# Kernel tuning notes

Measured on AMD Instinct MI355X. Metric: run time of the kernel, lower is better.

Reference implementation:

```python
import jax, jax.numpy as jnp
import numpy as np

NUM_TOKENS = 2048
HIDDEN = 1024
INTER = 2048
NUM_EXPERTS = 8
TOPK = 2


def setup_inputs() -> dict:
    key = jax.random.key(0)
    k1, k2, k3, k4 = jax.random.split(key, 4)
    hidden_states = jax.random.normal(k1, (NUM_TOKENS, HIDDEN), dtype=jnp.float32)
    router_logits = jax.random.normal(k2, (NUM_TOKENS, NUM_EXPERTS), dtype=jnp.float32)
    # fc1: [E, hidden, 2*intermediate] (proj/gate for SwiGLU), fc2: [E, intermediate, hidden]
    w1 = jax.random.normal(k3, (NUM_EXPERTS, HIDDEN, 2 * INTER), dtype=jnp.float32) * 0.02
    w2 = jax.random.normal(k4, (NUM_EXPERTS, INTER, HIDDEN), dtype=jnp.float32) * 0.02
    return {"hidden_states": hidden_states, "router_logits": router_logits, "w1": w1, "w2": w2}


def _grouped_gemm(x, w, expert_ids):
    """x: [T, D], w: [E, D, O], expert_ids: [T] -> [T, O].
    Tokens are routed to expert expert_ids[t]; equivalent to the sequential
    per-expert GEMM on contiguously sorted tokens. Small fixed loop over E."""
    out = jnp.zeros((x.shape[0], w.shape[-1]), dtype=x.dtype)
    for e in range(w.shape[0]):
        mask = (expert_ids == e)[:, None]
        out = out + jnp.where(mask, x, 0.0) @ w[e]
    return out


def reference(hidden_states, router_logits, w1, w2):
    # top-k routing + softmax over the selected logits
    top_logits, top_idx = jax.lax.top_k(router_logits, TOPK)      # [N, K]
    scores = jax.nn.softmax(top_logits, axis=-1)                  # [N, K]

    flat_idx = top_idx.reshape(-1)                                # [N*K]
    sorted_indices = jnp.argsort(flat_idx)                        # permute tokens grouped by expert
    permuted = hidden_states[sorted_indices // TOPK]              # [N*K, D]
    sorted_experts = flat_idx[sorted_indices]                     # [N*K] expert id per permuted row

    fc1_out = _grouped_gemm(permuted, w1, sorted_experts)         # [N*K, 2*I]
    proj, gate = jnp.split(fc1_out, 2, axis=-1)
    act = jax.nn.silu(proj) * gate                                # SwiGLU
    expert_out = _grouped_gemm(act, w2, sorted_experts)           # [N*K, D]

    # unpermute (scatter back) and weighted combine over top-k
    unpermuted = jnp.zeros_like(expert_out).at[sorted_indices].set(expert_out)
    unpermuted = unpermuted.reshape(-1, TOPK, expert_out.shape[-1])
    return (unpermuted * scores[..., None]).sum(axis=1)           # [N, D]
```

## Files before the change

kernel.cpp:

```cpp
#include <hip/hip_runtime.h>
#include <hip/hip_bf16.h>

constexpr int T = 2048;
constexpr int H = 1024;
constexpr int I = 2048;
constexpr int N2 = 2 * I;
constexpr int RCAP = 5120;
constexpr int MAXT = 40;

constexpr int WS_OFF = 16;
constexpr int WS_TEXP = 32;
constexpr int WS_TOPKP = 4256;
constexpr int WS_ROWTOK = 8352;
constexpr int WS_TOKROW = 13472;
constexpr size_t WSB_ZROW = 114688;
constexpr size_t WSB_HSB  = 131072;
constexpr size_t WSB_ACT  = 8u << 20;
constexpr size_t WSB_PW1  = 32u << 20;
constexpr size_t WSB_PW2  = 96u << 20;

constexpr int W1T_BLKS = 8 * 32 * 16;
constexpr int W2T_BLKS = 8 * 64 * 4;
constexpr int HSB_BLKS = T * H / 2048;
constexpr int FC1_BLKS = 32 * MAXT;

typedef __attribute__((ext_vector_type(4))) float f32x4;
typedef __attribute__((ext_vector_type(8))) short s16x8;

__device__ __forceinline__ short f2bf(float f) {
    unsigned u = __float_as_uint(f);
    u += 0x7FFFu + ((u >> 16) & 1u);
    return (short)(u >> 16);
}

#define MFMA16(a, b, c) __builtin_amdgcn_mfma_f32_16x16x32_bf16(a, b, c, 0, 0, 0)

__device__ __forceinline__ void gl2lds16(const void* g, void* l) {
    __builtin_amdgcn_global_load_lds(
        (const __attribute__((address_space(1))) void*)g,
        (__attribute__((address_space(3))) void*)l, 16, 0, 0);
}

#define VM_WAIT4 asm volatile("s_waitcnt vmcnt(4)" ::: "memory")
#define VM_WAIT0 asm volatile("s_waitcnt vmcnt(0)" ::: "memory")
#define BARRIER                                     \
    do {                                            \
        asm volatile("" ::: "memory");              \
        __builtin_amdgcn_s_barrier();               \
        asm volatile("" ::: "memory");              \
    } while (0)

__global__ __launch_bounds__(256) void pre_kernel(const float* __restrict__ logits,
                                                  int* __restrict__ wsi,
                                                  float* __restrict__ wsf,
                                                  const float* __restrict__ hs,
                                                  unsigned short* __restrict__ hsb,
                                                  const float* __restrict__ w1,
                                                  unsigned short* __restrict__ pw1) {
    __shared__ __align__(16) float Lf[32 * 256];
    const int t = threadIdx.x;

    if (blockIdx.x < W1T_BLKS) {
        int b = blockIdx.x;
        int cs = b & 15, k0i = (b >> 4) & 31, e = b >> 9;
        const float* src = w1 + (size_t)e * H * N2 + (size_t)(k0i * 32) * N2 + cs * 256;
        #pragma unroll
        for (int i = 0; i < 8; i++) {
            int c = t + i * 256;
            int row = c >> 6, col4 = (c & 63) * 4;
            gl2lds16(src + (size_t)row * N2 + col4, &Lf[c * 4]);
        }
        __syncthreads();
        int gatebit = cs >> 3, csl = cs & 7;
        #pragma unroll
        for (int i = 0; i < 4; i++) {
            int cidx = t + i * 256;
            int within = cidx & 31, subh = (cidx >> 5) & 1;
            int kg = (cidx >> 6) & 3, ctp = cidx >> 8;
            int x = ctp * 64 + subh * 32 + within;
            s16x8 s;
            #pragma unroll
            for (int kk = 0; kk < 8; kk++) s[kk] = f2bf(Lf[(kg * 8 + kk) * 256 + x]);
            int n = gatebit * 32 + subh * 64 + within;
            int ct = csl * 4 + ctp;
            *(s16x8*)(pw1 + ((size_t)(e * 32 + ct) * 32 + k0i) * 4096 + (kg * 128 + n) * 8) = s;
        }
        return;
    }
    if (blockIdx.x > W1T_BLKS) {
        int i = (((int)blockIdx.x - W1T_BLKS - 1) * 256 + t) * 8;
        f32x4 a = *(const f32x4*)(hs + i);
        f32x4 b = *(const f32x4*)(hs + i + 4);
        s16x8 s = {f2bf(a[0]), f2bf(a[1]), f2bf(a[2]), f2bf(a[3]),
                   f2bf(b[0]), f2bf(b[1]), f2bf(b[2]), f2bf(b[3])};
        *(s16x8*)(hsb + i) = s;
        return;
    }

    int* cnt  = (int*)Lf;
    int* base = cnt + 8;
    int* fill = base + 9;
    if (t < 8) { cnt[t] = 0; fill[t] = 0; }
    for (int r = t; r < RCAP; r += 256) wsi[WS_ROWTOK + r] = -1;
    unsigned short* zr = (unsigned short*)((char*)wsi + WSB_ZROW);
    for (int i = t; i < H; i += 256) zr[i] = 0;
    __syncthreads();

    int e0a[8], e1a[8];
    #pragma unroll
    for (int j = 0; j < 8; j++) {
        int tok = t * 8 + j;
        const float* l = logits + tok * 8;
        float v0 = -1e30f; int i0 = 0;
        #pragma unroll
        for (int i = 0; i < 8; i++) { float v = l[i]; if (v > v0) { v0 = v; i0 = i; } }
        float v1 = -1e30f; int i1 = 0;
        #pragma unroll
        for (int i = 0; i < 8; i++) { if (i == i0) continue; float v = l[i]; if (v > v1) { v1 = v; i1 = i; } }
        float ex = __expf(v1 - v0);
        float inv = 1.f / (1.f + ex);
        wsf[WS_TOPKP + tok * 2] = inv;
        wsf[WS_TOPKP + tok * 2 + 1] = ex * inv;
        e0a[j] = i0; e1a[j] = i1;
        atomicAdd(&cnt[i0], 1);
        atomicAdd(&cnt[i1], 1);
    }
    __syncthreads();
    if (t == 0) {
        int acc = 0;
        for (int e = 0; e < 8; e++) { base[e] = acc; acc += (cnt[e] + 127) & ~127; }
        base[8] = acc;
        for (int e = 0; e < 9; e++) wsi[WS_OFF + e] = base[e];
    }
    __syncthreads();
    for (int tt = t; tt < MAXT; tt += 256) {
        int rb = tt * 128, ex = 0;
        for (int e = 0; e < 8; e++)
            if (rb >= base[e] && rb < base[e + 1]) ex = e;
        wsi[WS_TEXP + tt] = ex;
    }
    #pragma unroll
    for (int j = 0; j < 8; j++) {
        int tok = t * 8 + j;
        int ee[2] = {e0a[j], e1a[j]};
        #pragma unroll
        for (int k = 0; k < 2; k++) {
            int e = ee[k];
            int slot = atomicAdd(&fill[e], 1);
            int r = base[e] + slot;
            wsi[WS_ROWTOK + r] = tok;
            wsi[WS_TOKROW + tok * 2 + k] = r;
        }
    }
}

__global__ __launch_bounds__(256, 4) void fc1_kernel(
    const unsigned short* __restrict__ hsb, const unsigned short* __restrict__ pw1,
    const int* __restrict__ wsi, const unsigned short* __restrict__ zrow,
    unsigned short* __restrict__ act,
    const float* __restrict__ w2, unsigned short* __restrict__ pw2) {
    __shared__ __align__(16) unsigned short SM[32 * 512];
    const int t = threadIdx.x;

    if (blockIdx.x >= FC1_BLKS) {
        float* Lf = (float*)SM;
        int b = (int)blockIdx.x - FC1_BLKS;
        int cs = b & 3, k0i = (b >> 2) & 63, e = b >> 8;
        const float* src = w2 + (size_t)e * I * H + (size_t)(k0i * 32) * H + cs * 256;
        #pragma unroll
        for (int i = 0; i < 8; i++) {
            int c = t + i * 256;
            int row = c >> 6, col4 = (c & 63) * 4;
            gl2lds16(src + (size_t)row * H + col4, &Lf[c * 4]);
        }
        __syncthreads();
        #pragma unroll
        for (int i = 0; i < 4; i++) {
            int cidx = t + i * 256;
            int n = cidx & 127, kg = (cidx >> 7) & 3, h1 = cidx >> 9;
            int x = h1 * 128 + n;
            s16x8 s;
            #pragma unroll
            for (int kk = 0; kk < 8; kk++) s[kk] = f2bf(Lf[(kg * 8 + kk) * 256 + x]);
            int ht = cs * 2 + h1;
            *(s16x8*)(pw2 + ((size_t)(e * 8 + ht) * 64 + k0i) * 4096 + (kg * 128 + n) * 8) = s;
        }
        return;
    }

    unsigned short* A0 = SM;
    unsigned short* B0 = SM + 4096;
    unsigned short* A1 = SM + 8192;
    unsigned short* B1 = SM + 12288;
    const int ct = blockIdx.x & 31, rt = blockIdx.x >> 5;
    const int rowb = rt * 128;
    if (rowb >= wsi[WS_OFF + 8]) return;
    const int e = wsi[WS_TEXP + rt];
    const unsigned short* pb = pw1 + (size_t)((e * 32 + ct) * 32) * 4096;

    const int m = t & 127;
    const int tok = wsi[WS_ROWTOK + rowb + m];
    const unsigned short* rp = (tok >= 0) ? (hsb + (size_t)tok * H) : zrow;
    const int kga = t >> 7;

    const int lane = t & 63, w = t >> 6, wr = w >> 1, wc = w & 1;
    const int q = lane >> 4, l16 = lane & 15;

    f32x4 zero = {0.f, 0.f, 0.f, 0.f};
    f32x4 acc[4][4];
    #pragma unroll
    for (int mi = 0; mi < 4; mi++)
        #pragma unroll
        for (int ni = 0; ni < 4; ni++) acc[mi][ni] = zero;

    #define FC1_STAGE(k0i, Ab, Bb)                                             \
        do {                                                                   \
            const int k0_ = (k0i) * 32;                                        \
            gl2lds16(rp + k0_ + kga * 8, &(Ab)[t * 8]);                        \
            gl2lds16(rp + k0_ + (kga + 2) * 8, &(Ab)[(t + 256) * 8]);          \
            const unsigned short* ps_ = pb + (size_t)(k0i) * 4096;             \
            gl2lds16(ps_ + t * 8, &(Bb)[t * 8]);                               \
            gl2lds16(ps_ + (t + 256) * 8, &(Bb)[(t + 256) * 8]);               \
        } while (0)

    #define FC1_COMPUTE(Ab, Bb)                                                \
        do {                                                                   \
            s16x8 af[4], bf[4];                                                \
            _Pragma("unroll")                                                  \
            for (int mi = 0; mi < 4; mi++)                                     \
                af[mi] = *(const s16x8*)&(Ab)[(q * 128 + wr * 64 + mi * 16 + l16) * 8]; \
            _Pragma("unroll")                                                  \
            for (int ni = 0; ni < 4; ni++)                                     \
                bf[ni] = *(const s16x8*)&(Bb)[(q * 128 + wc * 64 + ni * 16 + l16) * 8]; \
            _Pragma("unroll")                                                  \
            for (int mi = 0; mi < 4; mi++)                                     \
                _Pragma("unroll")                                              \
                for (int ni = 0; ni < 4; ni++)                                 \
                    acc[mi][ni] = MFMA16(af[mi], bf[ni], acc[mi][ni]);         \
        } while (0)

    FC1_STAGE(0, A0, B0);
    FC1_STAGE(1, A1, B1);
    for (int k0i = 0; k0i < 30; k0i += 2) {
        VM_WAIT4;
        BARRIER;
        FC1_COMPUTE(A0, B0);
        BARRIER;
        FC1_STAGE(k0i + 2, A0, B0);
        VM_WAIT4;
        BARRIER;
        FC1_COMPUTE(A1, B1);
        BARRIER;
        FC1_STAGE(k0i + 3, A1, B1);
    }
    VM_WAIT4;
    BARRIER;
    FC1_COMPUTE(A0, B0);
    BARRIER;
    VM_WAIT0;
    BARRIER;
    FC1_COMPUTE(A1, B1);

    #pragma unroll
    for (int mi = 0; mi < 4; mi++)
        #pragma unroll
        for (int r = 0; r < 4; r++) {
            int row = rowb + wr * 64 + mi * 16 + q * 4 + r;
            #pragma unroll
            for (int ni = 0; ni < 2; ni++) {
                int col = ct * 64 + wc * 32 + ni * 16 + l16;
                float p = acc[mi][ni][r], g = acc[mi][ni + 2][r];
                float val = p * g / (1.f + __expf(-p));
                act[(size_t)row * I + col] = (unsigned short)f2bf(val);
            }
        }
}

__global__ __launch_bounds__(256, 4) void fc2_kernel(
    const unsigned short* __restrict__ act, const unsigned short* __restrict__ pw2,
    const int* __restrict__ wsi, float* __restrict__ eo) {
    __shared__ __align__(16) unsigned short SM[32 * 512];
    unsigned short* A0 = SM;
    unsigned short* B0 = SM + 4096;
    unsigned short* A1 = SM + 8192;
    unsigned short* B1 = SM + 12288;
    const int t = threadIdx.x;
    const int ht = blockIdx.x, rt = blockIdx.y, ks = blockIdx.z;
    const int rowb = rt * 128;
    if (rowb >= wsi[WS_OFF + 8]) return;
    const int e = wsi[WS_TEXP + rt];
    const unsigned short* pb = pw2 + (size_t)((e * 8 + ht) * 64) * 4096;

    const int m = t & 127;
    const unsigned short* rp = act + (size_t)(rowb + m) * I;
    const int kga = t >> 7;

    const int lane = t & 63, w = t >> 6, wr = w >> 1, wc = w & 1;
    const int q = lane >> 4, l16 = lane & 15;

    f32x4 zero = {0.f, 0.f, 0.f, 0.f};
    f32x4 acc[4][4];
    #pragma unroll
    for (int mi = 0; mi < 4; mi++)
        #pragma unroll
        for (int ni = 0; ni < 4; ni++) acc[mi][ni] = zero;

    #define FC2_STAGE(k0i, Ab, Bb)                                             \
        do {                                                                   \
            const int k0_ = (k0i) * 32;                                        \
            gl2lds16(rp + k0_ + kga * 8, &(Ab)[t * 8]);                        \
            gl2lds16(rp + k0_ + (kga + 2) * 8, &(Ab)[(t + 256) * 8]);          \
            const unsigned short* ps_ = pb + (size_t)(k0i) * 4096;             \
            gl2lds16(ps_ + t * 8, &(Bb)[t * 8]);                               \
            gl2lds16(ps_ + (t + 256) * 8, &(Bb)[(t + 256) * 8]);               \
        } while (0)

    #define FC2_COMPUTE(Ab, Bb)                                                \
        do {                                                                   \
            s16x8 af[4], bf[4];                                                \
            _Pragma("unroll")                                                  \
            for (int mi = 0; mi < 4; mi++)                                     \
                af[mi] = *(const s16x8*)&(Ab)[(q * 128 + wr * 64 + mi * 16 + l16) * 8]; \
            _Pragma("unroll")                                                  \
            for (int ni = 0; ni < 4; ni++)                                     \
                bf[ni] = *(const s16x8*)&(Bb)[(q * 128 + wc * 64 + ni * 16 + l16) * 8]; \
            _Pragma("unroll")                                                  \
            for (int mi = 0; mi < 4; mi++)                                     \
                _Pragma("unroll")                                              \
                for (int ni = 0; ni < 4; ni++)                                 \
                    acc[mi][ni] = MFMA16(af[mi], bf[ni], acc[mi][ni]);         \
        } while (0)

    const int kb = ks * 32;
    FC2_STAGE(kb, A0, B0);
    FC2_STAGE(kb + 1, A1, B1);
    for (int j = 0; j < 30; j += 2) {
        VM_WAIT4;
        BARRIER;
        FC2_COMPUTE(A0, B0);
        BARRIER;
        FC2_STAGE(kb + j + 2, A0, B0);
        VM_WAIT4;
        BARRIER;
        FC2_COMPUTE(A1, B1);
        BARRIER;
        FC2_STAGE(kb + j + 3, A1, B1);
    }
    VM_WAIT4;
    BARRIER;
    FC2_COMPUTE(A0, B0);
    BARRIER;
    VM_WAIT0;
    BARRIER;
    FC2_COMPUTE(A1, B1);

    float* ed = eo + (size_t)ks * RCAP * H;
    #pragma unroll
    for (int mi = 0; mi < 4; mi++)
        #pragma unroll
        for (int r = 0; r < 4; r++) {
            int row = rowb + wr * 64 + mi * 16 + q * 4 + r;
            #pragma unroll
            for (int ni = 0; ni < 4; ni++) {
                int col = ht * 128 + wc * 64 + ni * 16 + l16;
                ed[(size_t)row * H + col] = acc[mi][ni][r];
            }
        }
}

__global__ __launch_bounds__(256) void combine_kernel(
    const float* __restrict__ eo, const int* __restrict__ wsi,
    const float* __restrict__ wsf, float* __restrict__ out) {
    const int tok = blockIdx.x;
    const int r0 = wsi[WS_TOKROW + tok * 2], r1 = wsi[WS_TOKROW + tok * 2 + 1];
    const float s0 = wsf[WS_TOPKP + tok * 2], s1 = wsf[WS_TOPKP + tok * 2 + 1];
    const float* a0 = eo + (size_t)r0 * H;
    const float* a1 = eo + (size_t)RCAP * H + (size_t)r0 * H;
    const float* b0 = eo + (size_t)r1 * H;
    const float* b1 = eo + (size_t)RCAP * H + (size_t)r1 * H;
    const int c = threadIdx.x * 4;
    f32x4 va0 = *(const f32x4*)(a0 + c), va1 = *(const f32x4*)(a1 + c);
    f32x4 vb0 = *(const f32x4*)(b0 + c), vb1 = *(const f32x4*)(b1 + c);
    f32x4 r;
    #pragma unroll
    for (int i = 0; i < 4; i++) r[i] = s0 * (va0[i] + va1[i]) + s1 * (vb0[i] + vb1[i]);
    *(f32x4*)(out + (size_t)tok * H + c) = r;
}

extern "C" void kernel_launch(void* const* d_in, const int* in_sizes, int n_in,
                              void* d_out, int out_size, void* d_ws, size_t ws_size,
                              hipStream_t stream) {
    const float* hs     = (const float*)d_in[0];
    const float* logits = (const float*)d_in[1];
    const float* w1     = (const float*)d_in[2];
    const float* w2     = (const float*)d_in[3];
    float* out = (float*)d_out;
    int* wsi = (int*)d_ws;
    float* wsf = (float*)d_ws;
    unsigned short* zrow = (unsigned short*)((char*)d_ws + WSB_ZROW);
    unsigned short* hsb  = (unsigned short*)((char*)d_ws + WSB_HSB);
    unsigned short* act  = (unsigned short*)((char*)d_ws + WSB_ACT);
    unsigned short* pw1  = (unsigned short*)((char*)d_ws + WSB_PW1);
    unsigned short* pw2  = (unsigned short*)((char*)d_ws + WSB_PW2);
    float* eo = (float*)((char*)d_ws + WSB_PW1);

    pre_kernel<<<W1T_BLKS + 1 + HSB_BLKS, 256, 0, stream>>>(logits, wsi, wsf, hs, hsb, w1, pw1);
    fc1_kernel<<<FC1_BLKS + W2T_BLKS, 256, 0, stream>>>(hsb, pw1, wsi, zrow, act, w2, pw2);
    fc2_kernel<<<dim3(8, MAXT, 2), 256, 0, stream>>>(act, pw2, wsi, eo);
    combine_kernel<<<T, 256, 0, stream>>>(eo, wsi, wsf, out);
}
```

Measured before the change: 353.8 us.

## Load B weight fragments directly into registers, bypassing LDS in FC1/FC2

```diff
diff --git a/kernel.cpp b/kernel.cpp
--- a/kernel.cpp
+++ b/kernel.cpp
@@ -41,8 +41,9 @@
         (__attribute__((address_space(3))) void*)l, 16, 0, 0);
 }
 
-#define VM_WAIT4 asm volatile("s_waitcnt vmcnt(4)" ::: "memory")
+#define VM_WAIT6 asm volatile("s_waitcnt vmcnt(6)" ::: "memory")
 #define VM_WAIT0 asm volatile("s_waitcnt vmcnt(0)" ::: "memory")
+#define MEMFENCE asm volatile("" ::: "memory")
 #define BARRIER                                     \
     do {                                            \
         asm volatile("" ::: "memory");              \
@@ -154,12 +155,12 @@
     }
 }
 
-__global__ __launch_bounds__(256, 4) void fc1_kernel(
+__global__ __launch_bounds__(256, 3) void fc1_kernel(
     const unsigned short* __restrict__ hsb, const unsigned short* __restrict__ pw1,
     const int* __restrict__ wsi, const unsigned short* __restrict__ zrow,
     unsigned short* __restrict__ act,
     const float* __restrict__ w2, unsigned short* __restrict__ pw2) {
-    __shared__ __align__(16) unsigned short SM[32 * 512];
+    __shared__ __align__(16) unsigned short SM[16384];
     const int t = threadIdx.x;
 
     if (blockIdx.x >= FC1_BLKS) {
@@ -189,9 +190,7 @@
     }
 
     unsigned short* A0 = SM;
-    unsigned short* B0 = SM + 4096;
-    unsigned short* A1 = SM + 8192;
-    unsigned short* B1 = SM + 12288;
+    unsigned short* A1 = SM + 4096;
     const int ct = blockIdx.x & 31, rt = blockIdx.x >> 5;
     const int rowb = rt * 128;
     if (rowb >= wsi[WS_OFF + 8]) return;
@@ -205,6 +204,7 @@
 
     const int lane = t & 63, w = t >> 6, wr = w >> 1, wc = w & 1;
     const int q = lane >> 4, l16 = lane & 15;
+    const unsigned short* bbase = pb + (size_t)(q * 128 + wc * 64 + l16) * 8;
 
     f32x4 zero = {0.f, 0.f, 0.f, 0.f};
     f32x4 acc[4][4];
@@ -213,53 +213,57 @@
         #pragma unroll
         for (int ni = 0; ni < 4; ni++) acc[mi][ni] = zero;
 
-    #define FC1_STAGE(k0i, Ab, Bb)                                             \
+    s16x8 b0[4], b1[4];
+
+    #define FC1_STAGEA(k0i, Ab)                                                \
         do {                                                                   \
             const int k0_ = (k0i) * 32;                                        \
             gl2lds16(rp + k0_ + kga * 8, &(Ab)[t * 8]);                        \
             gl2lds16(rp + k0_ + (kga + 2) * 8, &(Ab)[(t + 256) * 8]);          \
-            const unsigned short* ps_ = pb + (size_t)(k0i) * 4096;             \
-            gl2lds16(ps_ + t * 8, &(Bb)[t * 8]);                               \
-            gl2lds16(ps_ + (t + 256) * 8, &(Bb)[(t + 256) * 8]);               \
-        } while (0)
-
-    #define FC1_COMPUTE(Ab, Bb)                                                \
-        do {                                                                   \
-            s16x8 af[4], bf[4];                                                \
+        } while (0)
+
+    #define FC1_LOADB(k0i, bv)                                                 \
+        do {                                                                   \
+            const unsigned short* bp_ = bbase + (size_t)(k0i) * 4096;          \
+            bv[0] = *(const s16x8*)(bp_);                                      \
+            bv[1] = *(const s16x8*)(bp_ + 128);                                \
+            bv[2] = *(const s16x8*)(bp_ + 256);                                \
+            bv[3] = *(const s16x8*)(bp_ + 384);                                \
+        } while (0)
+
+    #define FC1_COMPUTE(Ab, bv)                                                \
+        do {                                                                   \
+            s16x8 af[4];                                                       \
             _Pragma("unroll")                                                  \
             for (int mi = 0; mi < 4; mi++)                                     \
                 af[mi] = *(const s16x8*)&(Ab)[(q * 128 + wr * 64 + mi * 16 + l16) * 8]; \
-            _Pragma("unroll")                                                  \
-            for (int ni = 0; ni < 4; ni++)                                     \
-                bf[ni] = *(const s16x8*)&(Bb)[(q * 128 + wc * 64 + ni * 16 + l16) * 8]; \
+            __builtin_amdgcn_s_setprio(1);                                     \
             _Pragma("unroll")                                                  \
             for (int mi = 0; mi < 4; mi++)                                     \
                 _Pragma("unroll")                                              \
                 for (int ni = 0; ni < 4; ni++)                                 \
-                    acc[mi][ni] = MFMA16(af[mi], bf[ni], acc[mi][ni]);         \
-        } while (0)
-
-    FC1_STAGE(0, A0, B0);
-    FC1_STAGE(1, A1, B1);
-    for (int k0i = 0; k0i < 30; k0i += 2) {
-        VM_WAIT4;
+                    acc[mi][ni] = MFMA16(af[mi], bv[ni], acc[mi][ni]);         \
+            __builtin_amdgcn_s_setprio(0);                                     \
+        } while (0)
+
+    FC1_STAGEA(0, A0); FC1_LOADB(0, b0);
+    MEMFENCE;
+    FC1_STAGEA(1, A1); FC1_LOADB(1, b1);
+    for (int k = 0; k < 30; k += 2) {
+        VM_WAIT6; BARRIER;
+        FC1_COMPUTE(A0, b0);
         BARRIER;
-        FC1_COMPUTE(A0, B0);
+        FC1_STAGEA(k + 2, A0); FC1_LOADB(k + 2, b0);
+        VM_WAIT6; BARRIER;
+        FC1_COMPUTE(A1, b1);
         BARRIER;
-        FC1_STAGE(k0i + 2, A0, B0);
-        VM_WAIT4;
-        BARRIER;
-        FC1_COMPUTE(A1, B1);
-        BARRIER;
-        FC1_STAGE(k0i + 3, A1, B1);
-    }
-    VM_WAIT4;
+        FC1_STAGEA(k + 3, A1); FC1_LOADB(k + 3, b1);
+    }
+    VM_WAIT6; BARRIER;
+    FC1_COMPUTE(A0, b0);
     BARRIER;
-    FC1_COMPUTE(A0, B0);
-    BARRIER;
-    VM_WAIT0;
-    BARRIER;
-    FC1_COMPUTE(A1, B1);
+    VM_WAIT0; BARRIER;
+    FC1_COMPUTE(A1, b1);
 
     #pragma unroll
     for (int mi = 0; mi < 4; mi++)
@@ -276,14 +280,12 @@
         }
 }
 
-__global__ __launch_bounds__(256, 4) void fc2_kernel(
+__global__ __launch_bounds__(256, 3) void fc2_kernel(
     const unsigned short* __restrict__ act, const unsigned short* __restrict__ pw2,
     const int* __restrict__ wsi, float* __restrict__ eo) {
-    __shared__ __align__(16) unsigned short SM[32 * 512];
+    __shared__ __align__(16) unsigned short SM[8192];
     unsigned short* A0 = SM;
-    unsigned short* B0 = SM + 4096;
-    unsigned short* A1 = SM + 8192;
-    unsigned short* B1 = SM + 12288;
+    unsigned short* A1 = SM + 4096;
     const int t = threadIdx.x;
     const int ht = blockIdx.x, rt = blockIdx.y, ks = blockIdx.z;
     const int rowb = rt * 128;
@@ -297,6 +299,7 @@
 
     const int lane = t & 63, w = t >> 6, wr = w >> 1, wc = w & 1;
     const int q = lane >> 4, l16 = lane & 15;
+    const unsigned short* bbase = pb + (size_t)(q * 128 + wc * 64 + l16) * 8;
 
     f32x4 zero = {0.f, 0.f, 0.f, 0.f};
     f32x4 acc[4][4];
@@ -305,54 +308,58 @@
         #pragma unroll
         for (int ni = 0; ni < 4; ni++) acc[mi][ni] = zero;
 
-    #define FC2_STAGE(k0i, Ab, Bb)                                             \
+    s16x8 b0[4], b1[4];
+
+    #define FC2_STAGEA(k0i, Ab)                                                \
         do {                                                                   \
             const int k0_ = (k0i) * 32;                                        \
             gl2lds16(rp + k0_ + kga * 8, &(Ab)[t * 8]);                        \
             gl2lds16(rp + k0_ + (kga + 2) * 8, &(Ab)[(t + 256) * 8]);          \
-            const unsigned short* ps_ = pb + (size_t)(k0i) * 4096;             \
-            gl2lds16(ps_ + t * 8, &(Bb)[t * 8]);                               \
-            gl2lds16(ps_ + (t + 256) * 8, &(Bb)[(t + 256) * 8]);               \
-        } while (0)
-
-    #define FC2_COMPUTE(Ab, Bb)                                                \
-        do {                                                                   \
-            s16x8 af[4], bf[4];                                                \
+        } while (0)
+
+    #define FC2_LOADB(k0i, bv)                                                 \
+        do {                                                                   \
+            const unsigned short* bp_ = bbase + (size_t)(k0i) * 4096;          \
+            bv[0] = *(const s16x8*)(bp_);                                      \
+            bv[1] = *(const s16x8*)(bp_ + 128);                                \
+            bv[2] = *(const s16x8*)(bp_ + 256);                                \
+            bv[3] = *(const s16x8*)(bp_ + 384);                                \
+        } while (0)
+
+    #define FC2_COMPUTE(Ab, bv)                                                \
+        do {                                                                   \
+            s16x8 af[4];                                                       \
             _Pragma("unroll")                                                  \
             for (int mi = 0; mi < 4; mi++)                                     \
                 af[mi] = *(const s16x8*)&(Ab)[(q * 128 + wr * 64 + mi * 16 + l16) * 8]; \
-            _Pragma("unroll")                                                  \
-            for (int ni = 0; ni < 4; ni++)                                     \
-                bf[ni] = *(const s16x8*)&(Bb)[(q * 128 + wc * 64 + ni * 16 + l16) * 8]; \
+            __builtin_amdgcn_s_setprio(1);                                     \
             _Pragma("unroll")                                                  \
             for (int mi = 0; mi < 4; mi++)                                     \
                 _Pragma("unroll")                                              \
                 for (int ni = 0; ni < 4; ni++)                                 \
-                    acc[mi][ni] = MFMA16(af[mi], bf[ni], acc[mi][ni]);         \
+                    acc[mi][ni] = MFMA16(af[mi], bv[ni], acc[mi][ni]);         \
+            __builtin_amdgcn_s_setprio(0);                                     \
         } while (0)
 
     const int kb = ks * 32;
-    FC2_STAGE(kb, A0, B0);
-    FC2_STAGE(kb + 1, A1, B1);
+    FC2_STAGEA(kb, A0); FC2_LOADB(kb, b0);
+    MEMFENCE;
+    FC2_STAGEA(kb + 1, A1); FC2_LOADB(kb + 1, b1);
     for (int j = 0; j < 30; j += 2) {
-        VM_WAIT4;
+        VM_WAIT6; BARRIER;
+        FC2_COMPUTE(A0, b0);
         BARRIER;
-        FC2_COMPUTE(A0, B0);
+        FC2_STAGEA(kb + j + 2, A0); FC2_LOADB(kb + j + 2, b0);
+        VM_WAIT6; BARRIER;
+        FC2_COMPUTE(A1, b1);
         BARRIER;
-        FC2_STAGE(kb + j + 2, A0, B0);
-        VM_WAIT4;
-        BARRIER;
-        FC2_COMPUTE(A1, B1);
-        BARRIER;
-        FC2_STAGE(kb + j + 3, A1, B1);
-    }
-    VM_WAIT4;
+        FC2_STAGEA(kb + j + 3, A1); FC2_LOADB(kb + j + 3, b1);
+    }
+    VM_WAIT6; BARRIER;
+    FC2_COMPUTE(A0, b0);
     BARRIER;
-    FC2_COMPUTE(A0, B0);
-    BARRIER;
-    VM_WAIT0;
-    BARRIER;
-    FC2_COMPUTE(A1, B1);
+    VM_WAIT0; BARRIER;
+    FC2_COMPUTE(A1, b1);
 
     float* ed = eo + (size_t)ks * RCAP * H;
     #pragma unroll
```

Result: slower. 362.3 us (+2.4%).
